# Kernel optimization log

Hardware: AMD Instinct MI355X
Metric: run time of the kernel (lower is better)

## Reference

```python
import jax, jax.numpy as jnp
import numpy as np

N_NODES = 50000
N_EDGES = 800000
N_GRAPHS = 64
NEG_SLOPE = 0.01  # nn.LeakyReLU default


def setup_inputs() -> dict:
    key = jax.random.key(0)
    ks = jax.random.split(key, 10)
    x = jax.random.normal(ks[0], (N_NODES, 128), dtype=jnp.float32)
    edge_index = jax.random.randint(ks[1], (2, N_EDGES), 0, N_NODES, dtype=jnp.int32)
    # balanced, sorted graph assignment -> every one of the 64 graphs is non-empty
    batch = ((jnp.arange(N_NODES, dtype=jnp.int32) * N_GRAPHS) // N_NODES).astype(jnp.int32)

    def lin(k, fan_in, fan_out):
        lim = 1.0 / np.sqrt(fan_in)
        return jax.random.uniform(k, (fan_in, fan_out), jnp.float32, -lim, lim)

    return {
        "x": x, "edge_index": edge_index, "batch": batch,
        "W1": lin(ks[2], 128, 64),   "b1": jnp.zeros((64,), jnp.float32),
        "W2": lin(ks[3], 64, 128),   "b2": jnp.zeros((128,), jnp.float32),
        "W3": lin(ks[4], 128, 256),  "b3": jnp.zeros((256,), jnp.float32),
        "Wc1": lin(ks[5], 256, 1024), "bc1": jnp.zeros((1024,), jnp.float32),
        "Wc2": lin(ks[6], 1024, 512), "bc2": jnp.zeros((512,), jnp.float32),
        "Wc3": lin(ks[7], 512, 4),    "bc3": jnp.zeros((4,), jnp.float32),
    }


def _gcn_conv(x, W, b, src, dst, dinv, n):
    """PyG GCNConv: add self-loops, sym-normalize, X W then scatter-add."""
    h = x @ W                                   # [N, out]
    norm = (dinv[src] * dinv[dst])[:, None]     # per-edge coefficient
    out = jax.ops.segment_sum(h[src] * norm, dst, num_segments=n)
    out = out + h * (dinv * dinv)[:, None]      # self-loop contribution
    return out + b


def reference(x, edge_index, batch, W1, b1, W2, b2, W3, b3,
              Wc1, bc1, Wc2, bc2, Wc3, bc3):
    n = x.shape[0]
    src, dst = edge_index[0], edge_index[1]
    # degrees with self-loops (edge weights = 1); shared by all three convs
    deg = jnp.zeros((n,), x.dtype).at[dst].add(1.0) + 1.0
    dinv = jax.lax.rsqrt(deg)

    leaky = lambda v: jnp.where(v >= 0, v, NEG_SLOPE * v)

    h = leaky(_gcn_conv(x, W1, b1, src, dst, dinv, n))   # [N, 64]
    h = leaky(_gcn_conv(h, W2, b2, src, dst, dinv, n))   # [N, 128]
    h = _gcn_conv(h, W3, b3, src, dst, dinv, n)          # [N, 256]

    g = jax.ops.segment_max(h, batch, num_segments=N_GRAPHS)  # [G, 256]

    g = jax.nn.relu(g @ Wc1 + bc1)
    g = jax.nn.relu(g @ Wc2 + bc2)
    return g @ Wc3 + bc3                                  # [G, 4]
```

## Files before the change

kernel.cpp:

```cpp
#include <hip/hip_runtime.h>
#include <math.h>

#define NN 50000
#define NE 800000
#define NG 64
#define NEG 0.01f

__device__ __forceinline__ unsigned fenc(float f) {
  unsigned b = __float_as_uint(f);
  return (b & 0x80000000u) ? ~b : (b | 0x80000000u);
}
__device__ __forceinline__ float fdec(unsigned k) {
  unsigned b = (k & 0x80000000u) ? (k ^ 0x80000000u) : ~k;
  return __uint_as_float(b);
}

__global__ void hist_kernel(const int* __restrict__ dst, int* __restrict__ cnt) {
  int i = blockIdx.x * blockDim.x + threadIdx.x;
  if (i < NE) atomicAdd(&cnt[dst[i]], 1);
}

#define SCAN_ELE 512
#define SCAN_NB ((NN + SCAN_ELE - 1) / SCAN_ELE)

__global__ __launch_bounds__(256) void scan_reduce(const int* __restrict__ cnt,
                                                   int* __restrict__ partials) {
  int b = blockIdx.x, t = threadIdx.x;
  int i = b * SCAN_ELE + t * 2;
  int v0 = (i < NN) ? cnt[i] : 0;
  int v1 = (i + 1 < NN) ? cnt[i + 1] : 0;
  __shared__ int red[256];
  red[t] = v0 + v1;
  __syncthreads();
  for (int ofs = 128; ofs > 0; ofs >>= 1) {
    if (t < ofs) red[t] += red[t + ofs];
    __syncthreads();
  }
  if (t == 0) partials[b] = red[0];
}

__global__ void scan_partials(int* __restrict__ partials) {
  __shared__ int s[128];
  int t = threadIdx.x;
  int v = (t < SCAN_NB) ? partials[t] : 0;
  s[t] = v;
  __syncthreads();
  for (int ofs = 1; ofs < 128; ofs <<= 1) {
    int u = (t >= ofs) ? s[t - ofs] : 0;
    __syncthreads();
    s[t] += u;
    __syncthreads();
  }
  if (t < SCAN_NB) partials[t] = s[t] - v;
}

__global__ __launch_bounds__(256) void scan_write(const int* __restrict__ cnt,
                                                  const int* __restrict__ partials,
                                                  int* __restrict__ row_start,
                                                  int* __restrict__ cursor,
                                                  float* __restrict__ dinv) {
  int b = blockIdx.x, t = threadIdx.x;
  int i = b * SCAN_ELE + t * 2;
  int v0 = (i < NN) ? cnt[i] : 0;
  int v1 = (i + 1 < NN) ? cnt[i + 1] : 0;
  int s = v0 + v1;
  __shared__ int sc[256];
  sc[t] = s;
  __syncthreads();
  for (int ofs = 1; ofs < 256; ofs <<= 1) {
    int u = (t >= ofs) ? sc[t - ofs] : 0;
    __syncthreads();
    sc[t] += u;
    __syncthreads();
  }
  int base = partials[b] + sc[t] - s;
  if (i < NN) {
    row_start[i] = base; cursor[i] = base;
    dinv[i] = 1.0f / sqrtf((float)(v0 + 1));
  }
  if (i + 1 < NN) {
    row_start[i + 1] = base + v0; cursor[i + 1] = base + v0;
    dinv[i + 1] = 1.0f / sqrtf((float)(v1 + 1));
  }
  if (b == SCAN_NB - 1 && t == 255) row_start[NN] = partials[b] + sc[255];
}

__global__ void scatter_kernel(const int* __restrict__ src, const int* __restrict__ dst,
                               int* __restrict__ cursor, int* __restrict__ csr) {
  int i = blockIdx.x * blockDim.x + threadIdx.x;
  if (i < NE) {
    int d = dst[i];
    int pos = atomicAdd(&cursor[d], 1);
    csr[pos] = src[i];
  }
}

template <int BN, int MODE>
__global__ __launch_bounds__(256) void gemm_big(const float* __restrict__ A,
                                                const float* __restrict__ B,
                                                const float* __restrict__ bias,
                                                const float* __restrict__ dinv,
                                                float* __restrict__ C,
                                                int M, int N, int K) {
  constexpr int TN = BN / 16;
  __shared__ float As[16][132];
  __shared__ float Bs[16][BN];
  const int t = threadIdx.x;
  const int tx = t & 15, ty = t >> 4;
  const int bm = blockIdx.y * 128, bn = blockIdx.x * BN;
  const int ar = t >> 2, ac = (t & 3) * 4;
  const int r0 = bm + ar, r1 = r0 + 64;
  const bool ok0 = r0 < M, ok1 = r1 < M;
  float acc[8][TN] = {};
  for (int k0 = 0; k0 < K; k0 += 16) {
    float4 a0 = ok0 ? *(const float4*)(A + (size_t)r0 * K + k0 + ac) : make_float4(0.f,0.f,0.f,0.f);
    float4 a1 = ok1 ? *(const float4*)(A + (size_t)r1 * K + k0 + ac) : make_float4(0.f,0.f,0.f,0.f);
    float4 bv0, bv1;
    if (BN == 128) {
      const int kr = t >> 5, c4 = (t & 31) * 4;
      bv0 = *(const float4*)(B + (size_t)(k0 + kr) * N + bn + c4);
      bv1 = *(const float4*)(B + (size_t)(k0 + kr + 8) * N + bn + c4);
    } else {
      const int kr = t >> 4, c4 = (t & 15) * 4;
      bv0 = *(const float4*)(B + (size_t)(k0 + kr) * N + bn + c4);
      bv1 = make_float4(0.f,0.f,0.f,0.f);
    }
    __syncthreads();
    As[ac + 0][ar] = a0.x; As[ac + 1][ar] = a0.y; As[ac + 2][ar] = a0.z; As[ac + 3][ar] = a0.w;
    As[ac + 0][ar + 64] = a1.x; As[ac + 1][ar + 64] = a1.y;
    As[ac + 2][ar + 64] = a1.z; As[ac + 3][ar + 64] = a1.w;
    if (BN == 128) {
      *(float4*)&Bs[t >> 5][(t & 31) * 4] = bv0;
      *(float4*)&Bs[(t >> 5) + 8][(t & 31) * 4] = bv1;
    } else {
      *(float4*)&Bs[t >> 4][(t & 15) * 4] = bv0;
    }
    __syncthreads();
#pragma unroll
    for (int k = 0; k < 16; ++k) {
      float a[8], b[TN];
      *(float4*)&a[0] = *(const float4*)&As[k][ty * 8];
      *(float4*)&a[4] = *(const float4*)&As[k][ty * 8 + 4];
      *(float4*)&b[0] = *(const float4*)&Bs[k][tx * 4];
      if (TN == 8) *(float4*)&b[4] = *(const float4*)&Bs[k][64 + tx * 4];
#pragma unroll
      for (int i = 0; i < 8; ++i)
#pragma unroll
        for (int j = 0; j < TN; ++j) acc[i][j] = fmaf(a[i], b[j], acc[i][j]);
    }
  }
  float bb[TN];
#pragma unroll
  for (int j = 0; j < TN; ++j) bb[j] = 0.f;
  if (MODE >= 1) {
#pragma unroll
    for (int j = 0; j < 4; ++j) bb[j] = bias[bn + tx * 4 + j];
    if (TN == 8)
#pragma unroll
      for (int j = 0; j < 4; ++j) bb[4 + j] = bias[bn + 64 + tx * 4 + j];
  }
#pragma unroll
  for (int i = 0; i < 8; ++i) {
    const int r = bm + ty * 8 + i;
    if (r < M) {
      const float dn = (MODE <= 1) ? dinv[r] : 1.0f;
      float v[TN];
#pragma unroll
      for (int j = 0; j < TN; ++j) {
        float u = acc[i][j] + bb[j];
        if (MODE == 1) u = (u >= 0.f) ? u : NEG * u;
        if (MODE <= 1) u = u * dn;
        v[j] = u;
      }
      *(float4*)(C + (size_t)r * N + bn + tx * 4) = make_float4(v[0], v[1], v[2], v[3]);
      if (TN == 8)
        *(float4*)(C + (size_t)r * N + bn + 64 + tx * 4) = make_float4(v[4], v[5], v[6], v[7]);
    }
  }
}

template <int MODE>
__global__ __launch_bounds__(256) void gemm_tile(const float* __restrict__ A,
                                                 const float* __restrict__ B,
                                                 const float* __restrict__ bias,
                                                 float* __restrict__ C,
                                                 int M, int N, int K) {
  __shared__ float As[16][68];
  __shared__ float Bs[16][64];
  const int t = threadIdx.x;
  const int tx = t & 15, ty = t >> 4;
  const int bm = blockIdx.y * 64, bn = blockIdx.x * 64;
  const int ar = t >> 2, ac = (t & 3) * 4;
  const int br = t >> 4, bc = (t & 15) * 4;
  const int arow = bm + ar;
  const bool aok = arow < M;
  float acc[4][4] = {};
  for (int k0 = 0; k0 < K; k0 += 16) {
    float4 a4 = aok ? *(const float4*)(A + (size_t)arow * K + k0 + ac)
                    : make_float4(0.f, 0.f, 0.f, 0.f);
    float4 b4 = *(const float4*)(B + (size_t)(k0 + br) * N + bn + bc);
    __syncthreads();
    As[ac + 0][ar] = a4.x;
    As[ac + 1][ar] = a4.y;
    As[ac + 2][ar] = a4.z;
    As[ac + 3][ar] = a4.w;
    *(float4*)&Bs[br][bc] = b4;
    __syncthreads();
#pragma unroll
    for (int k = 0; k < 16; ++k) {
      float a[4], b[4];
      *(float4*)a = *(const float4*)&As[k][ty * 4];
      *(float4*)b = *(const float4*)&Bs[k][tx * 4];
#pragma unroll
      for (int i = 0; i < 4; ++i)
#pragma unroll
        for (int j = 0; j < 4; ++j) acc[i][j] = fmaf(a[i], b[j], acc[i][j]);
    }
  }
  float bb[4] = {0.f, 0.f, 0.f, 0.f};
  if (MODE > 0) {
#pragma unroll
    for (int j = 0; j < 4; ++j) bb[j] = bias[bn + tx * 4 + j];
  }
#pragma unroll
  for (int i = 0; i < 4; ++i) {
    int r = bm + ty * 4 + i;
    if (r < M) {
      float vv[4];
#pragma unroll
      for (int j = 0; j < 4; ++j) {
        float v = acc[i][j] + bb[j];
        if (MODE == 3) v = fmaxf(v, 0.f);
        vv[j] = v;
      }
      *(float4*)(C + (size_t)r * N + bn + tx * 4) = make_float4(vv[0], vv[1], vv[2], vv[3]);
    }
  }
}

template <int MODE>
__global__ __launch_bounds__(256) void agg64_kernel(const float* __restrict__ hs,
                                                    const float* __restrict__ dinv,
                                                    const int* __restrict__ row_start,
                                                    const int* __restrict__ csr,
                                                    const float* __restrict__ bias,
                                                    float* __restrict__ out) {
  int wid = (blockIdx.x * 256 + threadIdx.x) >> 6;
  int lane = threadIdx.x & 63;
  if (wid >= NN) return;
  int e0 = row_start[wid], e1 = row_start[wid + 1];
  float a0 = 0.f, a1 = 0.f, a2 = 0.f, a3 = 0.f;
  int e = e0;
  for (; e + 4 <= e1; e += 4) {
    int s0 = csr[e], s1 = csr[e + 1], s2 = csr[e + 2], s3 = csr[e + 3];
    a0 += hs[(size_t)s0 * 64 + lane];
    a1 += hs[(size_t)s1 * 64 + lane];
    a2 += hs[(size_t)s2 * 64 + lane];
    a3 += hs[(size_t)s3 * 64 + lane];
  }
  for (; e < e1; ++e) a0 += hs[(size_t)csr[e] * 64 + lane];
  float dn = dinv[wid];
  float acc = (a0 + a1) + (a2 + a3) + hs[(size_t)wid * 64 + lane];
  float v = dn * acc;
  if (MODE == 1) {
    v += bias[lane];
    v = (v >= 0.f) ? v : NEG * v;
    v *= dn;
  }
  out[(size_t)wid * 64 + lane] = v;
}

__global__ __launch_bounds__(256) void agg128_kernel(const float* __restrict__ hs,
                                                     const float* __restrict__ dinv,
                                                     const int* __restrict__ row_start,
                                                     const int* __restrict__ csr,
                                                     float* __restrict__ out) {
  int wid = (blockIdx.x * 256 + threadIdx.x) >> 6;
  int lane = threadIdx.x & 63;
  if (wid >= NN) return;
  const float2* h2 = (const float2*)hs;
  int e0 = row_start[wid], e1 = row_start[wid + 1];
  float x0 = 0.f, y0 = 0.f, x1 = 0.f, y1 = 0.f, x2 = 0.f, y2 = 0.f, x3 = 0.f, y3 = 0.f;
  int e = e0;
  for (; e + 4 <= e1; e += 4) {
    int s0 = csr[e], s1 = csr[e + 1], s2 = csr[e + 2], s3 = csr[e + 3];
    float2 v0 = h2[(size_t)s0 * 64 + lane];
    float2 v1 = h2[(size_t)s1 * 64 + lane];
    float2 v2 = h2[(size_t)s2 * 64 + lane];
    float2 v3 = h2[(size_t)s3 * 64 + lane];
    x0 += v0.x; y0 += v0.y; x1 += v1.x; y1 += v1.y;
    x2 += v2.x; y2 += v2.y; x3 += v3.x; y3 += v3.y;
  }
  for (; e < e1; ++e) {
    float2 v = h2[(size_t)csr[e] * 64 + lane];
    x0 += v.x; y0 += v.y;
  }
  float2 self = h2[(size_t)wid * 64 + lane];
  float dn = dinv[wid];
  float2 o;
  o.x = dn * ((x0 + x1) + (x2 + x3) + self.x);
  o.y = dn * ((y0 + y1) + (y2 + y3) + self.y);
  ((float2*)out)[(size_t)wid * 64 + lane] = o;
}

#define SEG_CHUNK 125
__global__ __launch_bounds__(256) void segmax_kernel(const float* __restrict__ h,
                                                     const int* __restrict__ batch,
                                                     unsigned* __restrict__ gmax) {
  int t = threadIdx.x;
  int n0 = blockIdx.x * SEG_CHUNK;
  int n1 = n0 + SEG_CHUNK; if (n1 > NN) n1 = NN;
  int cur = batch[n0];
  float m = -INFINITY;
  for (int n = n0; n < n1; ++n) {
    int g = batch[n];
    if (g != cur) {
      atomicMax(&gmax[cur * 256 + t], fenc(m));
      cur = g;
      m = -INFINITY;
    }
    m = fmaxf(m, h[(size_t)n * 256 + t]);
  }
  atomicMax(&gmax[cur * 256 + t], fenc(m));
}

__global__ void decode_kernel(const unsigned* __restrict__ gmax, float* __restrict__ g) {
  int i = blockIdx.x * blockDim.x + threadIdx.x;
  if (i < NG * 256) g[i] = fdec(gmax[i]);
}

__global__ __launch_bounds__(256) void final_kernel(const float* __restrict__ g2,
                                                    const float* __restrict__ W,
                                                    const float* __restrict__ b,
                                                    float* __restrict__ out) {
  __shared__ float red[256][4];
  int m = blockIdx.x, t = threadIdx.x;
  float acc[4] = {0.f, 0.f, 0.f, 0.f};
  for (int k = t; k < 512; k += 256) {
    float gv = g2[m * 512 + k];
#pragma unroll
    for (int n = 0; n < 4; ++n) acc[n] = fmaf(gv, W[k * 4 + n], acc[n]);
  }
#pragma unroll
  for (int n = 0; n < 4; ++n) red[t][n] = acc[n];
  __syncthreads();
  for (int s = 128; s > 0; s >>= 1) {
    if (t < s)
#pragma unroll
      for (int n = 0; n < 4; ++n) red[t][n] += red[t + s][n];
    __syncthreads();
  }
  if (t < 4) out[m * 4 + t] = red[0][t] + b[t];
}

extern "C" void kernel_launch(void* const* d_in, const int* in_sizes, int n_in,
                              void* d_out, int out_size, void* d_ws, size_t ws_size,
                              hipStream_t stream) {
  const float* x   = (const float*)d_in[0];
  const int*   ei  = (const int*)d_in[1];
  const int* batch = (const int*)d_in[2];
  const float* W1  = (const float*)d_in[3];
  const float* b1  = (const float*)d_in[4];
  const float* W2  = (const float*)d_in[5];
  const float* b2  = (const float*)d_in[6];
  const float* W3  = (const float*)d_in[7];
  const float* b3  = (const float*)d_in[8];
  const float* Wc1 = (const float*)d_in[9];
  const float* bc1 = (const float*)d_in[10];
  const float* Wc2 = (const float*)d_in[11];
  const float* bc2 = (const float*)d_in[12];
  const float* Wc3 = (const float*)d_in[13];
  const float* bc3 = (const float*)d_in[14];
  const int* src = ei;
  const int* dst = ei + NE;

  char* base = (char*)d_ws;
  size_t off = 0;
  auto take = [&](size_t bytes) {
    size_t o = off;
    off += (bytes + 255) & ~(size_t)255;
    return o;
  };
  int*      deg_cnt   = (int*)(base + take((size_t)NN * 4));
  float*    dinv      = (float*)(base + take((size_t)NN * 4));
  int*      row_start = (int*)(base + take((size_t)(NN + 1) * 4));
  int*      cursor    = (int*)(base + take((size_t)NN * 4));
  int*      partials  = (int*)(base + take((size_t)SCAN_NB * 4));
  int*      csr       = (int*)(base + take((size_t)NE * 4));
  unsigned* gmax      = (unsigned*)(base + take((size_t)NG * 256 * 4));
  float*    gdec      = (float*)(base + take((size_t)NG * 256 * 4));
  float*    c1out     = (float*)(base + take((size_t)NG * 1024 * 4));
  float*    c2out     = (float*)(base + take((size_t)NG * 512 * 4));
  float* B64_a  = (float*)(base + take((size_t)NN * 64 * 4));
  float* B64_b  = (float*)(base + take((size_t)NN * 64 * 4));
  float* B128_a = (float*)(base + take((size_t)NN * 128 * 4));
  float* B128_b = (float*)(base + take((size_t)NN * 128 * 4));
  float* out3   = B64_a;

  hipMemsetAsync(deg_cnt, 0, (size_t)NN * 4, stream);
  hipMemsetAsync(gmax, 0, (size_t)NG * 256 * 4, stream);
  hist_kernel<<<(NE + 255) / 256, 256, 0, stream>>>(dst, deg_cnt);
  scan_reduce<<<SCAN_NB, 256, 0, stream>>>(deg_cnt, partials);
  scan_partials<<<1, 128, 0, stream>>>(partials);
  scan_write<<<SCAN_NB, 256, 0, stream>>>(deg_cnt, partials, row_start, cursor, dinv);
  scatter_kernel<<<(NE + 255) / 256, 256, 0, stream>>>(src, dst, cursor, csr);

  const int gy = (NN + 127) / 128;

  gemm_big<64, 0><<<dim3(1, gy), 256, 0, stream>>>(x, W1, nullptr, dinv, B64_a, NN, 64, 128);
  agg64_kernel<1><<<(NN * 64) / 256, 256, 0, stream>>>(B64_a, dinv, row_start, csr, b1, B64_b);

  agg64_kernel<0><<<(NN * 64) / 256, 256, 0, stream>>>(B64_b, dinv, row_start, csr, nullptr, B64_a);
  gemm_big<128, 1><<<dim3(1, gy), 256, 0, stream>>>(B64_a, W2, b2, dinv, B128_a, NN, 128, 64);

  agg128_kernel<<<(NN * 64) / 256, 256, 0, stream>>>(B128_a, dinv, row_start, csr, B128_b);
  gemm_big<128, 2><<<dim3(2, gy), 256, 0, stream>>>(B128_b, W3, b3, nullptr, out3, NN, 256, 128);

  segmax_kernel<<<(NN + SEG_CHUNK - 1) / SEG_CHUNK, 256, 0, stream>>>(out3, batch, gmax);
  decode_kernel<<<(NG * 256 + 255) / 256, 256, 0, stream>>>(gmax, gdec);
  gemm_tile<3><<<dim3(16, 1), 256, 0, stream>>>(gdec, Wc1, bc1, c1out, NG, 1024, 256);
  gemm_tile<3><<<dim3(8, 1), 256, 0, stream>>>(c1out, Wc2, bc2, c2out, NG, 512, 1024);
  final_kernel<<<NG, 256, 0, stream>>>(c2out, Wc3, bc3, (float*)d_out);
}
```

Measured before the change: 530.7 us.

## Fuse decode and three-layer classifier MLP into one per-graph kernel

Replaces the decode kernel, two tiled GEMM launches and the final reduction kernel with a single kernel that runs one block per graph. Each block decodes its max-pooled vector, then computes the three dense layers through shared memory. This removes three launches and the global round-trips of the intermediates. In exchange, each of the 64 blocks streams the full Wc1 and Wc2 weights with no cross-graph reuse, and the per-block work is serial over K (1024 iterations in the second layer), so this tail stage may take longer.

```diff
diff --git a/kernel.cpp b/kernel.cpp
--- a/kernel.cpp
+++ b/kernel.cpp
@@ -180,65 +180,6 @@
 }
 
 template <int MODE>
-__global__ __launch_bounds__(256) void gemm_tile(const float* __restrict__ A,
-                                                 const float* __restrict__ B,
-                                                 const float* __restrict__ bias,
-                                                 float* __restrict__ C,
-                                                 int M, int N, int K) {
-  __shared__ float As[16][68];
-  __shared__ float Bs[16][64];
-  const int t = threadIdx.x;
-  const int tx = t & 15, ty = t >> 4;
-  const int bm = blockIdx.y * 64, bn = blockIdx.x * 64;
-  const int ar = t >> 2, ac = (t & 3) * 4;
-  const int br = t >> 4, bc = (t & 15) * 4;
-  const int arow = bm + ar;
-  const bool aok = arow < M;
-  float acc[4][4] = {};
-  for (int k0 = 0; k0 < K; k0 += 16) {
-    float4 a4 = aok ? *(const float4*)(A + (size_t)arow * K + k0 + ac)
-                    : make_float4(0.f, 0.f, 0.f, 0.f);
-    float4 b4 = *(const float4*)(B + (size_t)(k0 + br) * N + bn + bc);
-    __syncthreads();
-    As[ac + 0][ar] = a4.x;
-    As[ac + 1][ar] = a4.y;
-    As[ac + 2][ar] = a4.z;
-    As[ac + 3][ar] = a4.w;
-    *(float4*)&Bs[br][bc] = b4;
-    __syncthreads();
-#pragma unroll
-    for (int k = 0; k < 16; ++k) {
-      float a[4], b[4];
-      *(float4*)a = *(const float4*)&As[k][ty * 4];
-      *(float4*)b = *(const float4*)&Bs[k][tx * 4];
-#pragma unroll
-      for (int i = 0; i < 4; ++i)
-#pragma unroll
-        for (int j = 0; j < 4; ++j) acc[i][j] = fmaf(a[i], b[j], acc[i][j]);
-    }
-  }
-  float bb[4] = {0.f, 0.f, 0.f, 0.f};
-  if (MODE > 0) {
-#pragma unroll
-    for (int j = 0; j < 4; ++j) bb[j] = bias[bn + tx * 4 + j];
-  }
-#pragma unroll
-  for (int i = 0; i < 4; ++i) {
-    int r = bm + ty * 4 + i;
-    if (r < M) {
-      float vv[4];
-#pragma unroll
-      for (int j = 0; j < 4; ++j) {
-        float v = acc[i][j] + bb[j];
-        if (MODE == 3) v = fmaxf(v, 0.f);
-        vv[j] = v;
-      }
-      *(float4*)(C + (size_t)r * N + bn + tx * 4) = make_float4(vv[0], vv[1], vv[2], vv[3]);
-    }
-  }
-}
-
-template <int MODE>
 __global__ __launch_bounds__(256) void agg64_kernel(const float* __restrict__ hs,
                                                     const float* __restrict__ dinv,
                                                     const int* __restrict__ row_start,
@@ -324,22 +265,60 @@
   atomicMax(&gmax[cur * 256 + t], fenc(m));
 }
 
-__global__ void decode_kernel(const unsigned* __restrict__ gmax, float* __restrict__ g) {
-  int i = blockIdx.x * blockDim.x + threadIdx.x;
-  if (i < NG * 256) g[i] = fdec(gmax[i]);
-}
-
-__global__ __launch_bounds__(256) void final_kernel(const float* __restrict__ g2,
-                                                    const float* __restrict__ W,
-                                                    const float* __restrict__ b,
-                                                    float* __restrict__ out) {
+__global__ __launch_bounds__(256) void mlp_kernel(const unsigned* __restrict__ gmax,
+                                                  const float* __restrict__ Wc1,
+                                                  const float* __restrict__ bc1,
+                                                  const float* __restrict__ Wc2,
+                                                  const float* __restrict__ bc2,
+                                                  const float* __restrict__ Wc3,
+                                                  const float* __restrict__ bc3,
+                                                  float* __restrict__ out) {
+  __shared__ float g0[256];
+  __shared__ float h1[1024];
+  __shared__ float h2[512];
   __shared__ float red[256][4];
-  int m = blockIdx.x, t = threadIdx.x;
+  const int b = blockIdx.x, t = threadIdx.x;
+
+  g0[t] = fdec(gmax[b * 256 + t]);
+  __syncthreads();
+
+  {
+    float4 acc = *(const float4*)(bc1 + 4 * t);
+#pragma unroll 8
+    for (int k = 0; k < 256; ++k) {
+      float gv = g0[k];
+      float4 w = *(const float4*)(Wc1 + (size_t)k * 1024 + 4 * t);
+      acc.x = fmaf(gv, w.x, acc.x);
+      acc.y = fmaf(gv, w.y, acc.y);
+      acc.z = fmaf(gv, w.z, acc.z);
+      acc.w = fmaf(gv, w.w, acc.w);
+    }
+    h1[4 * t + 0] = fmaxf(acc.x, 0.f);
+    h1[4 * t + 1] = fmaxf(acc.y, 0.f);
+    h1[4 * t + 2] = fmaxf(acc.z, 0.f);
+    h1[4 * t + 3] = fmaxf(acc.w, 0.f);
+  }
+  __syncthreads();
+
+  {
+    float2 acc = *(const float2*)(bc2 + 2 * t);
+#pragma unroll 8
+    for (int k = 0; k < 1024; ++k) {
+      float hv = h1[k];
+      float2 w = *(const float2*)(Wc2 + (size_t)k * 512 + 2 * t);
+      acc.x = fmaf(hv, w.x, acc.x);
+      acc.y = fmaf(hv, w.y, acc.y);
+    }
+    h2[2 * t + 0] = fmaxf(acc.x, 0.f);
+    h2[2 * t + 1] = fmaxf(acc.y, 0.f);
+  }
+  __syncthreads();
+
   float acc[4] = {0.f, 0.f, 0.f, 0.f};
   for (int k = t; k < 512; k += 256) {
-    float gv = g2[m * 512 + k];
-#pragma unroll
-    for (int n = 0; n < 4; ++n) acc[n] = fmaf(gv, W[k * 4 + n], acc[n]);
+    float hv = h2[k];
+#pragma unroll
+    for (int n = 0; n < 4; ++n) acc[n] = fmaf(hv, Wc3[k * 4 + n], acc[n]);
   }
 #pragma unroll
   for (int n = 0; n < 4; ++n) red[t][n] = acc[n];
@@ -350,7 +329,7 @@
       for (int n = 0; n < 4; ++n) red[t][n] += red[t + s][n];
     __syncthreads();
   }
-  if (t < 4) out[m * 4 + t] = red[0][t] + b[t];
+  if (t < 4) out[b * 4 + t] = red[0][t] + bc3[t];
 }
 
 extern "C" void kernel_launch(void* const* d_in, const int* in_sizes, int n_in,
@@ -388,9 +367,6 @@
   int*      partials  = (int*)(base + take((size_t)SCAN_NB * 4));
   int*      csr       = (int*)(base + take((size_t)NE * 4));
   unsigned* gmax      = (unsigned*)(base + take((size_t)NG * 256 * 4));
-  float*    gdec      = (float*)(base + take((size_t)NG * 256 * 4));
-  float*    c1out     = (float*)(base + take((size_t)NG * 1024 * 4));
-  float*    c2out     = (float*)(base + take((size_t)NG * 512 * 4));
   float* B64_a  = (float*)(base + take((size_t)NN * 64 * 4));
   float* B64_b  = (float*)(base + take((size_t)NN * 64 * 4));
   float* B128_a = (float*)(base + take((size_t)NN * 128 * 4));
@@ -417,8 +393,5 @@
   gemm_big<128, 2><<<dim3(2, gy), 256, 0, stream>>>(B128_b, W3, b3, nullptr, out3, NN, 256, 128);
 
   segmax_kernel<<<(NN + SEG_CHUNK - 1) / SEG_CHUNK, 256, 0, stream>>>(out3, batch, gmax);
-  decode_kernel<<<(NG * 256 + 255) / 256, 256, 0, stream>>>(gmax, gdec);
-  gemm_tile<3><<<dim3(16, 1), 256, 0, stream>>>(gdec, Wc1, bc1, c1out, NG, 1024, 256);
-  gemm_tile<3><<<dim3(8, 1), 256, 0, stream>>>(c1out, Wc2, bc2, c2out, NG, 512, 1024);
-  final_kernel<<<NG, 256, 0, stream>>>(c2out, Wc3, bc3, (float*)d_out);
-}
+  mlp_kernel<<<NG, 256, 0, stream>>>(gmax, Wc1, bc1, Wc2, bc2, Wc3, bc3, (float*)d_out);
+}
```

Result: faster. 510.9 us (-3.7%).
